# Kernel tuning notes

Hardware: AMD Instinct MI355X
Metric: run time of the kernel (lower is better)

The kernel has to match this reference:

```python
import jax, jax.numpy as jnp
import numpy as np

N_TOKENS = 2048
HIDDEN = 2048
N_EXPERTS = 8
TOP_K = 2
D_FF = 1408  # per-expert SwiGLU intermediate size


def setup_inputs() -> dict:
    key = jax.random.key(0)
    k_h, k_g, k_wg, k_wu, k_wd = jax.random.split(key, 5)
    s_in = 1.0 / np.sqrt(HIDDEN)
    s_ff = 1.0 / np.sqrt(D_FF)
    return {
        "h": jax.random.normal(k_h, (N_TOKENS, HIDDEN), dtype=jnp.float32),
        "gate_w": jax.random.normal(k_g, (N_EXPERTS, HIDDEN), dtype=jnp.float32) * s_in,
        "w_gate": jax.random.normal(k_wg, (N_EXPERTS, HIDDEN, D_FF), dtype=jnp.float32) * s_in,
        "w_up": jax.random.normal(k_wu, (N_EXPERTS, HIDDEN, D_FF), dtype=jnp.float32) * s_in,
        "w_down": jax.random.normal(k_wd, (N_EXPERTS, D_FF, HIDDEN), dtype=jnp.float32) * s_ff,
    }


def reference(h, gate_w, w_gate, w_up, w_down):
    # --- gate: linear (fp32) + softmax + top-k (no renorm, as in source) ---
    logits = jnp.einsum("nd,ed->ne", h.astype(jnp.float32), gate_w.astype(jnp.float32))
    scores = jax.nn.softmax(logits, axis=-1)                 # [N, E]
    topk_weight, topk_idx = jax.lax.top_k(scores, TOP_K)     # [N, K], [N, K]

    # --- per-expert SwiGLU MLP applied densely, then gather selected experts ---
    # (same math as the per-expert grouped GEMM dispatch in the eager loop)
    g = jnp.einsum("nd,edf->enf", h, w_gate)                 # [E, N, F]
    u = jnp.einsum("nd,edf->enf", h, w_up)                   # [E, N, F]
    y = jnp.einsum("enf,efd->end", jax.nn.silu(g) * u, w_down)  # [E, N, D]

    # gather each token's top-k expert outputs: [N, K, D]
    y_tok = jnp.transpose(y, (1, 0, 2))                      # [N, E, D]
    sel = jnp.take_along_axis(y_tok, topk_idx[:, :, None], axis=1)

    # weighted combine
    out = jnp.einsum("nk,nkd->nd", topk_weight.astype(h.dtype), sel)
    return out
```

## Files before the change

### kernel.cpp

```cpp
#include <hip/hip_runtime.h>
#include <hip/hip_bf16.h>
#include <stdint.h>

#define N_TOK 2048
#define HID   2048
#define NEXP  8
#define DFF   1408

typedef __attribute__((ext_vector_type(8))) short short8;
typedef __attribute__((ext_vector_type(4))) float f32x4;

__device__ __forceinline__ unsigned short f2bf(float f) {
  union { float ff; uint32_t u; } v; v.ff = f;
  return (unsigned short)((v.u + 0x7FFFu + ((v.u >> 16) & 1u)) >> 16);
}

__device__ __forceinline__ void gl2lds16(const void* g, void* l) {
  __builtin_amdgcn_global_load_lds(
      (const __attribute__((address_space(1))) void*)g,
      (__attribute__((address_space(3))) void*)l, 16, 0, 0);
}

__global__ __launch_bounds__(256) void gate_topk_k(
    const float* __restrict__ h, const float* __restrict__ gw,
    int* __restrict__ cnt, int* __restrict__ topk_idx, float* __restrict__ topk_w)
{
  int token = blockIdx.x * 4 + (threadIdx.x >> 6);
  int lane  = threadIdx.x & 63;
  const float* hr = h + (size_t)token * HID;
  float acc[NEXP];
#pragma unroll
  for (int e = 0; e < NEXP; ++e) acc[e] = 0.f;
  for (int i = lane; i < HID; i += 64) {
    float hv = hr[i];
#pragma unroll
    for (int e = 0; e < NEXP; ++e) acc[e] = fmaf(hv, gw[e * HID + i], acc[e]);
  }
#pragma unroll
  for (int e = 0; e < NEXP; ++e) {
    float a = acc[e];
#pragma unroll
    for (int s = 32; s > 0; s >>= 1) a += __shfl_xor(a, s, 64);
    acc[e] = a;
  }
  if (lane == 0) {
    float m = acc[0];
#pragma unroll
    for (int e = 1; e < NEXP; ++e) m = fmaxf(m, acc[e]);
    float w[NEXP]; float s = 0.f;
#pragma unroll
    for (int e = 0; e < NEXP; ++e) { w[e] = __expf(acc[e] - m); s += w[e]; }
    float inv = 1.f / s;
    int i0 = 0; float b0 = acc[0];
#pragma unroll
    for (int e = 1; e < NEXP; ++e) if (acc[e] > b0) { b0 = acc[e]; i0 = e; }
    int i1 = -1; float b1 = -3.4e38f;
#pragma unroll
    for (int e = 0; e < NEXP; ++e) if (e != i0 && acc[e] > b1) { b1 = acc[e]; i1 = e; }
    topk_idx[token * 2 + 0] = i0;
    topk_idx[token * 2 + 1] = i1;
    topk_w[token * 2 + 0] = w[i0] * inv;
    topk_w[token * 2 + 1] = w[i1] * inv;
    atomicAdd(&cnt[i0], 1);
    atomicAdd(&cnt[i1], 1);
  }
}

__global__ void prefix_k(const int* __restrict__ cnt, int* __restrict__ offs,
                         int* __restrict__ cursor) {
  if (threadIdx.x == 0 && blockIdx.x == 0) {
    int s = 0;
    for (int e = 0; e < NEXP; ++e) { offs[e] = s; cursor[e] = s; s += cnt[e]; }
  }
}

__global__ __launch_bounds__(256) void scatter_k(
    const int* __restrict__ topk_idx, const float* __restrict__ topk_w,
    int* __restrict__ cursor, int* __restrict__ pair_token, float* __restrict__ pair_w,
    int* __restrict__ tok_slot)
{
  int n = blockIdx.x * 256 + threadIdx.x;
  if (n >= N_TOK) return;
#pragma unroll
  for (int k = 0; k < 2; ++k) {
    int e = topk_idx[n * 2 + k];
    int p = atomicAdd(&cursor[e], 1);
    pair_token[p] = n;
    pair_w[p] = topk_w[n * 2 + k];
    tok_slot[n * 2 + k] = p;
  }
}

__global__ __launch_bounds__(256) void convert_h_k(const float* __restrict__ src,
                                                   unsigned short* __restrict__ dst) {
  int i = blockIdx.x * 256 + threadIdx.x;
  float4 a = ((const float4*)src)[(size_t)i * 2];
  float4 b = ((const float4*)src)[(size_t)i * 2 + 1];
  unsigned short o[8] = {f2bf(a.x), f2bf(a.y), f2bf(a.z), f2bf(a.w),
                         f2bf(b.x), f2bf(b.y), f2bf(b.z), f2bf(b.w)};
  *(short8*)&dst[(size_t)i * 8] = *(const short8*)o;
}

__global__ __launch_bounds__(256) void transpose_k(const float* __restrict__ s1,
                                                   unsigned short* __restrict__ d1,
                                                   const float* __restrict__ s2,
                                                   unsigned short* __restrict__ d2,
                                                   int R, int C, int nz1)
{
  __shared__ unsigned short T[64 * 66];
  const size_t sl = (size_t)R * C;
  int z = blockIdx.z;
  const float* s; unsigned short* d;
  if (z < nz1) { s = s1 + (size_t)z * sl; d = d1 + (size_t)z * sl; }
  else { s = s2 + (size_t)(z - nz1) * sl; d = d2 + (size_t)(z - nz1) * sl; }
  const int rb = blockIdx.x * 64, cb = blockIdx.y * 64;
  const int t = threadIdx.x;
  const int tr = t >> 4, tc = (t & 15) * 4;
  const float* sp = s + (size_t)(rb + tr) * C + cb + tc;
#pragma unroll
  for (int i = 0; i < 4; ++i) {
    float4 v = *(const float4*)(sp + (size_t)i * 16 * C);
    int r = tr + i * 16;
    uint32_t p0 = (uint32_t)f2bf(v.x) | ((uint32_t)f2bf(v.y) << 16);
    uint32_t p1 = (uint32_t)f2bf(v.z) | ((uint32_t)f2bf(v.w) << 16);
    *(uint32_t*)&T[r * 66 + tc]     = p0;
    *(uint32_t*)&T[r * 66 + tc + 2] = p1;
  }
  __syncthreads();
  const int f = t >> 2, ch = (t & 3) * 16;
  unsigned short* dp = d + (size_t)(cb + f) * R + rb + ch;
#pragma unroll
  for (int g = 0; g < 2; ++g) {
    unsigned short buf[8];
#pragma unroll
    for (int j = 0; j < 8; ++j) buf[j] = T[(ch + g * 8 + j) * 66 + f];
    *(short8*)(dp + g * 8) = *(const short8*)buf;
  }
}

__global__ __launch_bounds__(512) void gateup4_k(
    const unsigned short* __restrict__ hbf,
    const unsigned short* __restrict__ wgt, const unsigned short* __restrict__ wut,
    const int* __restrict__ cnt, const int* __restrict__ offs,
    const int* __restrict__ pair_token, unsigned short* __restrict__ act,
    int e_fixed, int nw, int nbcnt, size_t wstride)
{
  const int x = blockIdx.x;
  const int wti = x % nw, mb = x / nw;
  int e, nb;
  if (e_fixed >= 0) { e = e_fixed; nb = wti; }
  else { e = wti / nbcnt; nb = wti % nbcnt; }
  const int count = cnt[e];
  if (mb * 128 >= count) return;
  const int off = offs[e];
  const int rows = min(128, count - mb * 128);
  const int c0 = nb * 128;

  __shared__ unsigned short As[128 * 64];
  __shared__ unsigned short Bg[128 * 64];
  __shared__ unsigned short Bu[128 * 64];
  __shared__ int tok[128];

  const int t = threadIdx.x;
  if (t < 128) tok[t] = pair_token[off + mb * 128 + min(t, rows - 1)];
  __syncthreads();

  const int w = t >> 6, l = t & 63;
  const int sr = l >> 3;
  const int sc = ((l & 7) ^ sr) * 8;
  const int r0 = w * 16 + sr, r1 = w * 16 + 8 + sr;

  const size_t wb = (e_fixed >= 0) ? 0 : (size_t)e * wstride;
  const unsigned short* wgE = wgt + wb;
  const unsigned short* wuE = wut + wb;
  const unsigned short* aP0 = hbf + (size_t)tok[r0] * HID + sc;
  const unsigned short* aP1 = hbf + (size_t)tok[r1] * HID + sc;
  const unsigned short* gP0 = wgE + (size_t)(c0 + r0) * HID + sc;
  const unsigned short* gP1 = wgE + (size_t)(c0 + r1) * HID + sc;
  const unsigned short* uP0 = wuE + (size_t)(c0 + r0) * HID + sc;
  const unsigned short* uP1 = wuE + (size_t)(c0 + r1) * HID + sc;
  const int ldsLo = (w * 16) * 64, ldsHi = (w * 16 + 8) * 64;

  const int fr = l & 15, fq = l >> 4;
  const int wr = (w >> 2) * 64, wc = (w & 3) * 32;
  const int f3 = fr & 7;

  f32x4 accg[4][2], accu[4][2];
#pragma unroll
  for (int i = 0; i < 4; ++i)
#pragma unroll
    for (int j = 0; j < 2; ++j) {
      accg[i][j] = (f32x4){0.f, 0.f, 0.f, 0.f};
      accu[i][j] = (f32x4){0.f, 0.f, 0.f, 0.f};
    }

  for (int kt = 0; kt < HID; kt += 64) {
    gl2lds16(aP0 + kt, &As[ldsLo]); gl2lds16(aP1 + kt, &As[ldsHi]);
    gl2lds16(gP0 + kt, &Bg[ldsLo]); gl2lds16(gP1 + kt, &Bg[ldsHi]);
    gl2lds16(uP0 + kt, &Bu[ldsLo]); gl2lds16(uP1 + kt, &Bu[ldsHi]);
    __syncthreads();

    short8 af[4][2], bg[2][2], bu[2][2];
#pragma unroll
    for (int kk = 0; kk < 2; ++kk) {
      const int ch = ((kk * 4 + fq) ^ f3) * 8;
#pragma unroll
      for (int mi = 0; mi < 4; ++mi)
        af[mi][kk] = *(const short8*)&As[(wr + mi * 16 + fr) * 64 + ch];
#pragma unroll
      for (int ni = 0; ni < 2; ++ni) {
        bg[ni][kk] = *(const short8*)&Bg[(wc + ni * 16 + fr) * 64 + ch];
        bu[ni][kk] = *(const short8*)&Bu[(wc + ni * 16 + fr) * 64 + ch];
      }
    }
#pragma unroll
    for (int kk = 0; kk < 2; ++kk)
#pragma unroll
      for (int mi = 0; mi < 4; ++mi)
#pragma unroll
        for (int ni = 0; ni < 2; ++ni) {
          accg[mi][ni] = __builtin_amdgcn_mfma_f32_16x16x32_bf16(af[mi][kk], bg[ni][kk], accg[mi][ni], 0, 0, 0);
          accu[mi][ni] = __builtin_amdgcn_mfma_f32_16x16x32_bf16(af[mi][kk], bu[ni][kk], accu[mi][ni], 0, 0, 0);
        }
    __syncthreads();
  }

#pragma unroll
  for (int mi = 0; mi < 4; ++mi)
#pragma unroll
    for (int ni = 0; ni < 2; ++ni)
#pragma unroll
      for (int j = 0; j < 4; ++j) {
        int r = wr + mi * 16 + fq * 4 + j;
        if (r < rows) {
          float g = accg[mi][ni][j], u = accu[mi][ni][j];
          float a = (g / (1.f + __expf(-g))) * u;
          act[(size_t)(off + mb * 128 + r) * DFF + (c0 + wc + ni * 16 + fr)] = f2bf(a);
        }
      }
}

__global__ __launch_bounds__(256) void down4_k(
    const unsigned short* __restrict__ act, const unsigned short* __restrict__ wdt,
    const int* __restrict__ cnt, const int* __restrict__ offs,
    float* __restrict__ ypair, int e_fixed, int nw, int nbcnt, size_t wstride)
{
  const int x = blockIdx.x;
  const int wti = x % nw, mb = x / nw;
  int e, nb;
  if (e_fixed >= 0) { e = e_fixed; nb = wti; }
  else { e = wti / nbcnt; nb = wti % nbcnt; }
  const int count = cnt[e];
  if (mb * 128 >= count) return;
  const int off = offs[e];
  const int rows = min(128, count - mb * 128);
  const int c0 = nb * 128;

  __shared__ unsigned short As[128 * 64];
  __shared__ unsigned short Bd[128 * 64];

  const int t = threadIdx.x;
  const int w = t >> 6, l = t & 63;
  const int sr = l >> 3;
  const int sc = ((l & 7) ^ sr) * 8;
  const size_t wb = (e_fixed >= 0) ? 0 : (size_t)e * wstride;
  const unsigned short* wdE = wdt + wb;

  const unsigned short* aP[4];
  const unsigned short* bP[4];
  int ldsB[4];
#pragma unroll
  for (int i = 0; i < 4; ++i) {
    int rr = w * 32 + i * 8 + sr;
    aP[i] = act + (size_t)(off + mb * 128 + rr) * DFF + sc;
    bP[i] = wdE + (size_t)(c0 + rr) * DFF + sc;
    ldsB[i] = (w * 32 + i * 8) * 64;
  }

  const int fr = l & 15, fq = l >> 4;
  const int wr = (w >> 1) * 64, wc = (w & 1) * 64;
  const int f3 = fr & 7;

  f32x4 acc[4][4];
#pragma unroll
  for (int i = 0; i < 4; ++i)
#pragma unroll
    for (int j = 0; j < 4; ++j) acc[i][j] = (f32x4){0.f, 0.f, 0.f, 0.f};

  for (int kt = 0; kt < DFF; kt += 64) {
#pragma unroll
    for (int i = 0; i < 4; ++i) {
      gl2lds16(aP[i] + kt, &As[ldsB[i]]);
      gl2lds16(bP[i] + kt, &Bd[ldsB[i]]);
    }
    __syncthreads();

    short8 af[4][2], bd[4][2];
#pragma unroll
    for (int kk = 0; kk < 2; ++kk) {
      const int ch = ((kk * 4 + fq) ^ f3) * 8;
#pragma unroll
      for (int mi = 0; mi < 4; ++mi)
        af[mi][kk] = *(const short8*)&As[(wr + mi * 16 + fr) * 64 + ch];
#pragma unroll
      for (int ni = 0; ni < 4; ++ni)
        bd[ni][kk] = *(const short8*)&Bd[(wc + ni * 16 + fr) * 64 + ch];
    }
#pragma unroll
    for (int kk = 0; kk < 2; ++kk)
#pragma unroll
      for (int mi = 0; mi < 4; ++mi)
#pragma unroll
        for (int ni = 0; ni < 4; ++ni)
          acc[mi][ni] = __builtin_amdgcn_mfma_f32_16x16x32_bf16(af[mi][kk], bd[ni][kk], acc[mi][ni], 0, 0, 0);
    __syncthreads();
  }

#pragma unroll
  for (int mi = 0; mi < 4; ++mi)
#pragma unroll
    for (int ni = 0; ni < 4; ++ni)
#pragma unroll
      for (int j = 0; j < 4; ++j) {
        int r = wr + mi * 16 + fq * 4 + j;
        if (r < rows)
          ypair[(size_t)(off + mb * 128 + r) * HID + (c0 + wc + ni * 16 + fr)] = acc[mi][ni][j];
      }
}

__global__ __launch_bounds__(256) void combine_k(
    const float* __restrict__ ypair, const int* __restrict__ tok_slot,
    const float* __restrict__ topk_w, float* __restrict__ out)
{
  int i = blockIdx.x * 256 + threadIdx.x;
  int n = i >> (11 - 2);
  int dv = (i & 511) * 4;
  int s0 = tok_slot[n * 2], s1 = tok_slot[n * 2 + 1];
  float w0 = topk_w[n * 2], w1 = topk_w[n * 2 + 1];
  float4 a = *(const float4*)&ypair[(size_t)s0 * HID + dv];
  float4 b = *(const float4*)&ypair[(size_t)s1 * HID + dv];
  float4 o;
  o.x = w0 * a.x + w1 * b.x; o.y = w0 * a.y + w1 * b.y;
  o.z = w0 * a.z + w1 * b.z; o.w = w0 * a.w + w1 * b.w;
  *(float4*)&out[(size_t)n * HID + dv] = o;
}

extern "C" void kernel_launch(void* const* d_in, const int* in_sizes, int n_in,
                              void* d_out, int out_size, void* d_ws, size_t ws_size,
                              hipStream_t stream) {
  const float* h  = (const float*)d_in[0];
  const float* gw = (const float*)d_in[1];
  const float* wg = (const float*)d_in[2];
  const float* wu = (const float*)d_in[3];
  const float* wd = (const float*)d_in[4];
  float* out = (float*)d_out;

  const size_t SL = (size_t)DFF * HID;
  char* ws = (char*)d_ws;
  int*   cnt        = (int*)(ws + 0);
  int*   offs       = (int*)(ws + 32);
  int*   cursor     = (int*)(ws + 64);
  int*   pair_token = (int*)(ws + 256);
  float* pair_w     = (float*)(ws + 16640);
  int*   tok_slot   = (int*)(ws + 33024);
  int*   topk_idx   = (int*)(ws + 49408);
  float* topk_w     = (float*)(ws + 65792);
  unsigned short* act = (unsigned short*)(ws + 82176);
  unsigned short* hbf = (unsigned short*)(ws + 11616512);
  unsigned short* wgt = (unsigned short*)(ws + 20005120);
  unsigned short* wut = (unsigned short*)(ws + 66142464);
  float* ypair_full   = (float*)(ws + 66142464);
  const size_t NEED_FULL = 112279808ull;

  hipMemsetAsync(ws, 0, 256, stream);

  gate_topk_k<<<N_TOK / 4, 256, 0, stream>>>(h, gw, cnt, topk_idx, topk_w);
  prefix_k<<<1, 64, 0, stream>>>(cnt, offs, cursor);
  scatter_k<<<N_TOK / 256, 256, 0, stream>>>(topk_idx, topk_w, cursor, pair_token, pair_w, tok_slot);
  convert_h_k<<<(N_TOK * HID / 8) / 256, 256, 0, stream>>>(h, hbf);

  if (ws_size >= NEED_FULL) {
    transpose_k<<<dim3(HID / 64, DFF / 64, 16), 256, 0, stream>>>(wg, wgt, wu, wut, HID, DFF, 8);
    gateup4_k<<<88 * 16, 512, 0, stream>>>(hbf, wgt, wut, cnt, offs, pair_token, act,
                                           -1, 88, 11, SL);
    transpose_k<<<dim3(DFF / 64, HID / 64, 8), 256, 0, stream>>>(wd, wgt, wd, wgt, DFF, HID, 8);
    down4_k<<<128 * 16, 256, 0, stream>>>(act, wgt, cnt, offs, ypair_full,
                                          -1, 128, 16, SL);
    combine_k<<<(N_TOK * HID / 4) / 256, 256, 0, stream>>>(ypair_full, tok_slot, topk_w, out);
  } else {
    unsigned short* wgtE = (unsigned short*)(ws + 20005120);
    unsigned short* wutE = (unsigned short*)(ws + 25772288);
    float* ypair = (float*)(ws + 31539456);
    for (int e = 0; e < NEXP; ++e) {
      transpose_k<<<dim3(HID / 64, DFF / 64, 2), 256, 0, stream>>>(wg + e * SL, wgtE, wu + e * SL, wutE, HID, DFF, 1);
      gateup4_k<<<11 * 16, 512, 0, stream>>>(hbf, wgtE, wutE, cnt, offs, pair_token, act,
                                             e, 11, 11, 0);
    }
    for (int e = 0; e < NEXP; ++e) {
      transpose_k<<<dim3(DFF / 64, HID / 64, 1), 256, 0, stream>>>(wd + e * SL, wgtE, wd + e * SL, wgtE, DFF, HID, 1);
      down4_k<<<16 * 16, 256, 0, stream>>>(act, wgtE, cnt, offs, ypair, e, 16, 16, 0);
    }
    combine_k<<<(N_TOK * HID / 4) / 256, 256, 0, stream>>>(ypair, tok_slot, topk_w, out);
  }
}
```

Baseline: 329.7 us.

## Double-buffer LDS tiles in grouped GEMM kernels with prefetch and MFMA priority

Both the gate/up and down grouped GEMM kernels now use two LDS buffers per operand. The next K tile is issued via global_load_lds before computing on the current one, with explicit vmcnt waits and barriers replacing __syncthreads. This overlaps global-to-LDS transfer with MFMA work, and s_setprio raises wave priority around the MFMA block. The cost is doubled LDS per block, which may lower occupancy, most notably for the 512-thread gate/up kernel at 96KB.

```diff
diff --git a/kernel.cpp b/kernel.cpp
--- a/kernel.cpp
+++ b/kernel.cpp
@@ -138,7 +138,7 @@
   }
 }
 
-__global__ __launch_bounds__(512) void gateup4_k(
+__global__ __launch_bounds__(512) void gateup5_k(
     const unsigned short* __restrict__ hbf,
     const unsigned short* __restrict__ wgt, const unsigned short* __restrict__ wut,
     const int* __restrict__ cnt, const int* __restrict__ offs,
@@ -156,9 +156,9 @@
   const int rows = min(128, count - mb * 128);
   const int c0 = nb * 128;
 
-  __shared__ unsigned short As[128 * 64];
-  __shared__ unsigned short Bg[128 * 64];
-  __shared__ unsigned short Bu[128 * 64];
+  __shared__ unsigned short As[2][128 * 64];
+  __shared__ unsigned short Bg[2][128 * 64];
+  __shared__ unsigned short Bu[2][128 * 64];
   __shared__ int tok[128];
 
   const int t = threadIdx.x;
@@ -194,25 +194,26 @@
       accu[i][j] = (f32x4){0.f, 0.f, 0.f, 0.f};
     }
 
-  for (int kt = 0; kt < HID; kt += 64) {
-    gl2lds16(aP0 + kt, &As[ldsLo]); gl2lds16(aP1 + kt, &As[ldsHi]);
-    gl2lds16(gP0 + kt, &Bg[ldsLo]); gl2lds16(gP1 + kt, &Bg[ldsHi]);
-    gl2lds16(uP0 + kt, &Bu[ldsLo]); gl2lds16(uP1 + kt, &Bu[ldsHi]);
-    __syncthreads();
-
+  auto stage = [&](int b, int kt) {
+    gl2lds16(aP0 + kt, &As[b][ldsLo]); gl2lds16(aP1 + kt, &As[b][ldsHi]);
+    gl2lds16(gP0 + kt, &Bg[b][ldsLo]); gl2lds16(gP1 + kt, &Bg[b][ldsHi]);
+    gl2lds16(uP0 + kt, &Bu[b][ldsLo]); gl2lds16(uP1 + kt, &Bu[b][ldsHi]);
+  };
+  auto compute = [&](int b) {
     short8 af[4][2], bg[2][2], bu[2][2];
 #pragma unroll
     for (int kk = 0; kk < 2; ++kk) {
       const int ch = ((kk * 4 + fq) ^ f3) * 8;
 #pragma unroll
       for (int mi = 0; mi < 4; ++mi)
-        af[mi][kk] = *(const short8*)&As[(wr + mi * 16 + fr) * 64 + ch];
+        af[mi][kk] = *(const short8*)&As[b][(wr + mi * 16 + fr) * 64 + ch];
 #pragma unroll
       for (int ni = 0; ni < 2; ++ni) {
-        bg[ni][kk] = *(const short8*)&Bg[(wc + ni * 16 + fr) * 64 + ch];
-        bu[ni][kk] = *(const short8*)&Bu[(wc + ni * 16 + fr) * 64 + ch];
+        bg[ni][kk] = *(const short8*)&Bg[b][(wc + ni * 16 + fr) * 64 + ch];
+        bu[ni][kk] = *(const short8*)&Bu[b][(wc + ni * 16 + fr) * 64 + ch];
       }
     }
+    __builtin_amdgcn_s_setprio(1);
 #pragma unroll
     for (int kk = 0; kk < 2; ++kk)
 #pragma unroll
@@ -222,8 +223,23 @@
           accg[mi][ni] = __builtin_amdgcn_mfma_f32_16x16x32_bf16(af[mi][kk], bg[ni][kk], accg[mi][ni], 0, 0, 0);
           accu[mi][ni] = __builtin_amdgcn_mfma_f32_16x16x32_bf16(af[mi][kk], bu[ni][kk], accu[mi][ni], 0, 0, 0);
         }
-    __syncthreads();
-  }
+    __builtin_amdgcn_s_setprio(0);
+  };
+
+  const int NK = HID / 64;
+  stage(0, 0);
+  int cur = 0;
+  for (int k = 0; k + 1 < NK; ++k) {
+    stage(cur ^ 1, (k + 1) * 64);
+    asm volatile("s_waitcnt vmcnt(6)" ::: "memory");
+    asm volatile("s_barrier" ::: "memory");
+    compute(cur);
+    asm volatile("s_barrier" ::: "memory");
+    cur ^= 1;
+  }
+  asm volatile("s_waitcnt vmcnt(0)" ::: "memory");
+  asm volatile("s_barrier" ::: "memory");
+  compute(cur);
 
 #pragma unroll
   for (int mi = 0; mi < 4; ++mi)
@@ -240,7 +256,7 @@
       }
 }
 
-__global__ __launch_bounds__(256) void down4_k(
+__global__ __launch_bounds__(256) void down5_k(
     const unsigned short* __restrict__ act, const unsigned short* __restrict__ wdt,
     const int* __restrict__ cnt, const int* __restrict__ offs,
     float* __restrict__ ypair, int e_fixed, int nw, int nbcnt, size_t wstride)
@@ -256,8 +272,8 @@
   const int rows = min(128, count - mb * 128);
   const int c0 = nb * 128;
 
-  __shared__ unsigned short As[128 * 64];
-  __shared__ unsigned short Bd[128 * 64];
+  __shared__ unsigned short As[2][128 * 64];
+  __shared__ unsigned short Bd[2][128 * 64];
 
   const int t = threadIdx.x;
   const int w = t >> 6, l = t & 63;
@@ -287,25 +303,26 @@
 #pragma unroll
     for (int j = 0; j < 4; ++j) acc[i][j] = (f32x4){0.f, 0.f, 0.f, 0.f};
 
-  for (int kt = 0; kt < DFF; kt += 64) {
+  auto stage = [&](int b, int kt) {
 #pragma unroll
     for (int i = 0; i < 4; ++i) {
-      gl2lds16(aP[i] + kt, &As[ldsB[i]]);
-      gl2lds16(bP[i] + kt, &Bd[ldsB[i]]);
-    }
-    __syncthreads();
-
+      gl2lds16(aP[i] + kt, &As[b][ldsB[i]]);
+      gl2lds16(bP[i] + kt, &Bd[b][ldsB[i]]);
+    }
+  };
+  auto compute = [&](int b) {
     short8 af[4][2], bd[4][2];
 #pragma unroll
     for (int kk = 0; kk < 2; ++kk) {
       const int ch = ((kk * 4 + fq) ^ f3) * 8;
 #pragma unroll
       for (int mi = 0; mi < 4; ++mi)
-        af[mi][kk] = *(const short8*)&As[(wr + mi * 16 + fr) * 64 + ch];
+        af[mi][kk] = *(const short8*)&As[b][(wr + mi * 16 + fr) * 64 + ch];
 #pragma unroll
       for (int ni = 0; ni < 4; ++ni)
-        bd[ni][kk] = *(const short8*)&Bd[(wc + ni * 16 + fr) * 64 + ch];
-    }
+        bd[ni][kk] = *(const short8*)&Bd[b][(wc + ni * 16 + fr) * 64 + ch];
+    }
+    __builtin_amdgcn_s_setprio(1);
 #pragma unroll
     for (int kk = 0; kk < 2; ++kk)
 #pragma unroll
@@ -313,8 +330,23 @@
 #pragma unroll
         for (int ni = 0; ni < 4; ++ni)
           acc[mi][ni] = __builtin_amdgcn_mfma_f32_16x16x32_bf16(af[mi][kk], bd[ni][kk], acc[mi][ni], 0, 0, 0);
-    __syncthreads();
-  }
+    __builtin_amdgcn_s_setprio(0);
+  };
+
+  const int NK = DFF / 64;
+  stage(0, 0);
+  int cur = 0;
+  for (int k = 0; k + 1 < NK; ++k) {
+    stage(cur ^ 1, (k + 1) * 64);
+    asm volatile("s_waitcnt vmcnt(8)" ::: "memory");
+    asm volatile("s_barrier" ::: "memory");
+    compute(cur);
+    asm volatile("s_barrier" ::: "memory");
+    cur ^= 1;
+  }
+  asm volatile("s_waitcnt vmcnt(0)" ::: "memory");
+  asm volatile("s_barrier" ::: "memory");
+  compute(cur);
 
 #pragma unroll
   for (int mi = 0; mi < 4; ++mi)
@@ -333,7 +365,7 @@
     const float* __restrict__ topk_w, float* __restrict__ out)
 {
   int i = blockIdx.x * 256 + threadIdx.x;
-  int n = i >> (11 - 2);
+  int n = i >> 9;
   int dv = (i & 511) * 4;
   int s0 = tok_slot[n * 2], s1 = tok_slot[n * 2 + 1];
   float w0 = topk_w[n * 2], w1 = topk_w[n * 2 + 1];
@@ -381,10 +413,10 @@
 
   if (ws_size >= NEED_FULL) {
     transpose_k<<<dim3(HID / 64, DFF / 64, 16), 256, 0, stream>>>(wg, wgt, wu, wut, HID, DFF, 8);
-    gateup4_k<<<88 * 16, 512, 0, stream>>>(hbf, wgt, wut, cnt, offs, pair_token, act,
+    gateup5_k<<<88 * 16, 512, 0, stream>>>(hbf, wgt, wut, cnt, offs, pair_token, act,
                                            -1, 88, 11, SL);
     transpose_k<<<dim3(DFF / 64, HID / 64, 8), 256, 0, stream>>>(wd, wgt, wd, wgt, DFF, HID, 8);
-    down4_k<<<128 * 16, 256, 0, stream>>>(act, wgt, cnt, offs, ypair_full,
+    down5_k<<<128 * 16, 256, 0, stream>>>(act, wgt, cnt, offs, ypair_full,
                                           -1, 128, 16, SL);
     combine_k<<<(N_TOK * HID / 4) / 256, 256, 0, stream>>>(ypair_full, tok_slot, topk_w, out);
   } else {
@@ -393,12 +425,12 @@
     float* ypair = (float*)(ws + 31539456);
     for (int e = 0; e < NEXP; ++e) {
       transpose_k<<<dim3(HID / 64, DFF / 64, 2), 256, 0, stream>>>(wg + e * SL, wgtE, wu + e * SL, wutE, HID, DFF, 1);
-      gateup4_k<<<11 * 16, 512, 0, stream>>>(hbf, wgtE, wutE, cnt, offs, pair_token, act,
+      gateup5_k<<<11 * 16, 512, 0, stream>>>(hbf, wgtE, wutE, cnt, offs, pair_token, act,
                                              e, 11, 11, 0);
     }
     for (int e = 0; e < NEXP; ++e) {
       transpose_k<<<dim3(DFF / 64, HID / 64, 1), 256, 0, stream>>>(wd + e * SL, wgtE, wd + e * SL, wgtE, DFF, HID, 1);
-      down4_k<<<16 * 16, 256, 0, stream>>>(act, wgtE, cnt, offs, ypair, e, 16, 16, 0);
+      down5_k<<<16 * 16, 256, 0, stream>>>(act, wgtE, cnt, offs, ypair, e, 16, 16, 0);
     }
     combine_k<<<(N_TOK * HID / 4) / 256, 256, 0, stream>>>(ypair, tok_slot, topk_w, out);
   }
```

After: 322.4 us. -2.2%, faster.

## Replace LDS-tiled expert GEMMs with single-wave direct-load MFMA kernels

Applied to the files above, without the earlier changes.

Both grouped GEMMs (gate/up with fused SwiGLU, and down) are rewritten as 64-thread single-wavefront kernels that load MFMA operands straight from global memory into registers. This drops LDS staging and block barriers. Tiles shrink to 64x32 and 64x64 per wave, and each block now loops over several row blocks with stride 8 instead of one block per row tile. This removes shared-memory and sync overhead and raises the number of independent waves, but loses LDS reuse across waves, so global/L2 traffic goes up and the direct loads are uncoalesced 16-byte row-strided accesses.

```diff
diff --git a/kernel.cpp b/kernel.cpp
--- a/kernel.cpp
+++ b/kernel.cpp
@@ -15,11 +15,7 @@
   return (unsigned short)((v.u + 0x7FFFu + ((v.u >> 16) & 1u)) >> 16);
 }
 
-__device__ __forceinline__ void gl2lds16(const void* g, void* l) {
-  __builtin_amdgcn_global_load_lds(
-      (const __attribute__((address_space(1))) void*)g,
-      (__attribute__((address_space(3))) void*)l, 16, 0, 0);
-}
+#define MFMA16(a, b, c) __builtin_amdgcn_mfma_f32_16x16x32_bf16((a), (b), (c), 0, 0, 0)
 
 __global__ __launch_bounds__(256) void gate_topk_k(
     const float* __restrict__ h, const float* __restrict__ gw,
@@ -138,7 +134,7 @@
   }
 }
 
-__global__ __launch_bounds__(512) void gateup4_k(
+__global__ __launch_bounds__(64) void gateup10_k(
     const unsigned short* __restrict__ hbf,
     const unsigned short* __restrict__ wgt, const unsigned short* __restrict__ wut,
     const int* __restrict__ cnt, const int* __restrict__ offs,
@@ -146,186 +142,155 @@
     int e_fixed, int nw, int nbcnt, size_t wstride)
 {
   const int x = blockIdx.x;
-  const int wti = x % nw, mb = x / nw;
+  const int wti = x % nw;
   int e, nb;
   if (e_fixed >= 0) { e = e_fixed; nb = wti; }
   else { e = wti / nbcnt; nb = wti % nbcnt; }
   const int count = cnt[e];
-  if (mb * 128 >= count) return;
   const int off = offs[e];
-  const int rows = min(128, count - mb * 128);
-  const int c0 = nb * 128;
-
-  __shared__ unsigned short As[128 * 64];
-  __shared__ unsigned short Bg[128 * 64];
-  __shared__ unsigned short Bu[128 * 64];
-  __shared__ int tok[128];
-
-  const int t = threadIdx.x;
-  if (t < 128) tok[t] = pair_token[off + mb * 128 + min(t, rows - 1)];
-  __syncthreads();
-
-  const int w = t >> 6, l = t & 63;
-  const int sr = l >> 3;
-  const int sc = ((l & 7) ^ sr) * 8;
-  const int r0 = w * 16 + sr, r1 = w * 16 + 8 + sr;
-
+  const int c0 = nb * 32;
+
+  const int l = threadIdx.x;
+  const int fr = l & 15, fq = l >> 4;
   const size_t wb = (e_fixed >= 0) ? 0 : (size_t)e * wstride;
-  const unsigned short* wgE = wgt + wb;
-  const unsigned short* wuE = wut + wb;
-  const unsigned short* aP0 = hbf + (size_t)tok[r0] * HID + sc;
-  const unsigned short* aP1 = hbf + (size_t)tok[r1] * HID + sc;
-  const unsigned short* gP0 = wgE + (size_t)(c0 + r0) * HID + sc;
-  const unsigned short* gP1 = wgE + (size_t)(c0 + r1) * HID + sc;
-  const unsigned short* uP0 = wuE + (size_t)(c0 + r0) * HID + sc;
-  const unsigned short* uP1 = wuE + (size_t)(c0 + r1) * HID + sc;
-  const int ldsLo = (w * 16) * 64, ldsHi = (w * 16 + 8) * 64;
-
-  const int fr = l & 15, fq = l >> 4;
-  const int wr = (w >> 2) * 64, wc = (w & 3) * 32;
-  const int f3 = fr & 7;
-
-  f32x4 accg[4][2], accu[4][2];
-#pragma unroll
-  for (int i = 0; i < 4; ++i)
-#pragma unroll
-    for (int j = 0; j < 2; ++j) {
-      accg[i][j] = (f32x4){0.f, 0.f, 0.f, 0.f};
-      accu[i][j] = (f32x4){0.f, 0.f, 0.f, 0.f};
-    }
-
-  for (int kt = 0; kt < HID; kt += 64) {
-    gl2lds16(aP0 + kt, &As[ldsLo]); gl2lds16(aP1 + kt, &As[ldsHi]);
-    gl2lds16(gP0 + kt, &Bg[ldsLo]); gl2lds16(gP1 + kt, &Bg[ldsHi]);
-    gl2lds16(uP0 + kt, &Bu[ldsLo]); gl2lds16(uP1 + kt, &Bu[ldsHi]);
-    __syncthreads();
-
-    short8 af[4][2], bg[2][2], bu[2][2];
-#pragma unroll
-    for (int kk = 0; kk < 2; ++kk) {
-      const int ch = ((kk * 4 + fq) ^ f3) * 8;
-#pragma unroll
-      for (int mi = 0; mi < 4; ++mi)
-        af[mi][kk] = *(const short8*)&As[(wr + mi * 16 + fr) * 64 + ch];
-#pragma unroll
-      for (int ni = 0; ni < 2; ++ni) {
-        bg[ni][kk] = *(const short8*)&Bg[(wc + ni * 16 + fr) * 64 + ch];
-        bu[ni][kk] = *(const short8*)&Bu[(wc + ni * 16 + fr) * 64 + ch];
+
+  const unsigned short* bgP0 = wgt + wb + (size_t)(c0 + fr) * HID + fq * 8;
+  const unsigned short* bgP1 = wgt + wb + (size_t)(c0 + 16 + fr) * HID + fq * 8;
+  const unsigned short* buP0 = wut + wb + (size_t)(c0 + fr) * HID + fq * 8;
+  const unsigned short* buP1 = wut + wb + (size_t)(c0 + 16 + fr) * HID + fq * 8;
+
+  for (int mb = x / nw; mb * 64 < count; mb += 8) {
+    const int m0 = mb * 64;
+    const int rows = min(64, count - m0);
+
+    const unsigned short* aP[4];
+#pragma unroll
+    for (int mi = 0; mi < 4; ++mi) {
+      int r = min(m0 + mi * 16 + fr, count - 1);
+      aP[mi] = hbf + (size_t)pair_token[off + r] * HID + fq * 8;
+    }
+
+    f32x4 accg[4][2], accu[4][2];
+#pragma unroll
+    for (int i = 0; i < 4; ++i)
+#pragma unroll
+      for (int j = 0; j < 2; ++j) {
+        accg[i][j] = (f32x4){0.f, 0.f, 0.f, 0.f};
+        accu[i][j] = (f32x4){0.f, 0.f, 0.f, 0.f};
       }
-    }
-#pragma unroll
-    for (int kk = 0; kk < 2; ++kk)
-#pragma unroll
-      for (int mi = 0; mi < 4; ++mi)
-#pragma unroll
-        for (int ni = 0; ni < 2; ++ni) {
-          accg[mi][ni] = __builtin_amdgcn_mfma_f32_16x16x32_bf16(af[mi][kk], bg[ni][kk], accg[mi][ni], 0, 0, 0);
-          accu[mi][ni] = __builtin_amdgcn_mfma_f32_16x16x32_bf16(af[mi][kk], bu[ni][kk], accu[mi][ni], 0, 0, 0);
+
+    for (int kt = 0; kt < HID; kt += 64) {
+      short8 a[4][2], bg[2][2], bu[2][2];
+#pragma unroll
+      for (int kk = 0; kk < 2; ++kk) {
+        const int ko = kt + kk * 32;
+#pragma unroll
+        for (int mi = 0; mi < 4; ++mi)
+          a[mi][kk] = *(const short8*)(aP[mi] + ko);
+        bg[0][kk] = *(const short8*)(bgP0 + ko);
+        bg[1][kk] = *(const short8*)(bgP1 + ko);
+        bu[0][kk] = *(const short8*)(buP0 + ko);
+        bu[1][kk] = *(const short8*)(buP1 + ko);
+      }
+#pragma unroll
+      for (int kk = 0; kk < 2; ++kk)
+#pragma unroll
+        for (int mi = 0; mi < 4; ++mi) {
+          accg[mi][0] = MFMA16(a[mi][kk], bg[0][kk], accg[mi][0]);
+          accg[mi][1] = MFMA16(a[mi][kk], bg[1][kk], accg[mi][1]);
+          accu[mi][0] = MFMA16(a[mi][kk], bu[0][kk], accu[mi][0]);
+          accu[mi][1] = MFMA16(a[mi][kk], bu[1][kk], accu[mi][1]);
         }
-    __syncthreads();
-  }
-
-#pragma unroll
-  for (int mi = 0; mi < 4; ++mi)
-#pragma unroll
-    for (int ni = 0; ni < 2; ++ni)
-#pragma unroll
-      for (int j = 0; j < 4; ++j) {
-        int r = wr + mi * 16 + fq * 4 + j;
-        if (r < rows) {
-          float g = accg[mi][ni][j], u = accu[mi][ni][j];
-          float a = (g / (1.f + __expf(-g))) * u;
-          act[(size_t)(off + mb * 128 + r) * DFF + (c0 + wc + ni * 16 + fr)] = f2bf(a);
+    }
+
+#pragma unroll
+    for (int mi = 0; mi < 4; ++mi)
+#pragma unroll
+      for (int ni = 0; ni < 2; ++ni)
+#pragma unroll
+        for (int j = 0; j < 4; ++j) {
+          int r = mi * 16 + fq * 4 + j;
+          if (r < rows) {
+            float g = accg[mi][ni][j], u = accu[mi][ni][j];
+            float a = (g / (1.f + __expf(-g))) * u;
+            act[(size_t)(off + m0 + r) * DFF + (c0 + ni * 16 + fr)] = f2bf(a);
+          }
         }
-      }
-}
-
-__global__ __launch_bounds__(256) void down4_k(
+  }
+}
+
+__global__ __launch_bounds__(64) void down10_k(
     const unsigned short* __restrict__ act, const unsigned short* __restrict__ wdt,
     const int* __restrict__ cnt, const int* __restrict__ offs,
     float* __restrict__ ypair, int e_fixed, int nw, int nbcnt, size_t wstride)
 {
   const int x = blockIdx.x;
-  const int wti = x % nw, mb = x / nw;
+  const int wti = x % nw;
   int e, nb;
   if (e_fixed >= 0) { e = e_fixed; nb = wti; }
   else { e = wti / nbcnt; nb = wti % nbcnt; }
   const int count = cnt[e];
-  if (mb * 128 >= count) return;
   const int off = offs[e];
-  const int rows = min(128, count - mb * 128);
-  const int c0 = nb * 128;
-
-  __shared__ unsigned short As[128 * 64];
-  __shared__ unsigned short Bd[128 * 64];
-
-  const int t = threadIdx.x;
-  const int w = t >> 6, l = t & 63;
-  const int sr = l >> 3;
-  const int sc = ((l & 7) ^ sr) * 8;
+  const int c0 = nb * 64;
+
+  const int l = threadIdx.x;
+  const int fr = l & 15, fq = l >> 4;
   const size_t wb = (e_fixed >= 0) ? 0 : (size_t)e * wstride;
-  const unsigned short* wdE = wdt + wb;
-
-  const unsigned short* aP[4];
-  const unsigned short* bP[4];
-  int ldsB[4];
-#pragma unroll
-  for (int i = 0; i < 4; ++i) {
-    int rr = w * 32 + i * 8 + sr;
-    aP[i] = act + (size_t)(off + mb * 128 + rr) * DFF + sc;
-    bP[i] = wdE + (size_t)(c0 + rr) * DFF + sc;
-    ldsB[i] = (w * 32 + i * 8) * 64;
-  }
-
-  const int fr = l & 15, fq = l >> 4;
-  const int wr = (w >> 1) * 64, wc = (w & 1) * 64;
-  const int f3 = fr & 7;
-
-  f32x4 acc[4][4];
-#pragma unroll
-  for (int i = 0; i < 4; ++i)
-#pragma unroll
-    for (int j = 0; j < 4; ++j) acc[i][j] = (f32x4){0.f, 0.f, 0.f, 0.f};
-
-  for (int kt = 0; kt < DFF; kt += 64) {
-#pragma unroll
-    for (int i = 0; i < 4; ++i) {
-      gl2lds16(aP[i] + kt, &As[ldsB[i]]);
-      gl2lds16(bP[i] + kt, &Bd[ldsB[i]]);
-    }
-    __syncthreads();
-
-    short8 af[4][2], bd[4][2];
-#pragma unroll
-    for (int kk = 0; kk < 2; ++kk) {
-      const int ch = ((kk * 4 + fq) ^ f3) * 8;
-#pragma unroll
-      for (int mi = 0; mi < 4; ++mi)
-        af[mi][kk] = *(const short8*)&As[(wr + mi * 16 + fr) * 64 + ch];
+
+  const unsigned short* bdP[4];
+#pragma unroll
+  for (int ni = 0; ni < 4; ++ni)
+    bdP[ni] = wdt + wb + (size_t)(c0 + ni * 16 + fr) * DFF + fq * 8;
+
+  for (int mb = x / nw; mb * 64 < count; mb += 8) {
+    const int m0 = mb * 64;
+    const int rows = min(64, count - m0);
+
+    const unsigned short* aP[4];
+#pragma unroll
+    for (int mi = 0; mi < 4; ++mi) {
+      int r = min(m0 + mi * 16 + fr, count - 1);
+      aP[mi] = act + (size_t)(off + r) * DFF + fq * 8;
+    }
+
+    f32x4 acc[4][4];
+#pragma unroll
+    for (int i = 0; i < 4; ++i)
+#pragma unroll
+      for (int j = 0; j < 4; ++j) acc[i][j] = (f32x4){0.f, 0.f, 0.f, 0.f};
+
+    for (int kt = 0; kt < DFF; kt += 64) {
+      short8 a[4][2], bd[4][2];
+#pragma unroll
+      for (int kk = 0; kk < 2; ++kk) {
+        const int ko = kt + kk * 32;
+#pragma unroll
+        for (int mi = 0; mi < 4; ++mi)
+          a[mi][kk] = *(const short8*)(aP[mi] + ko);
+#pragma unroll
+        for (int ni = 0; ni < 4; ++ni)
+          bd[ni][kk] = *(const short8*)(bdP[ni] + ko);
+      }
+#pragma unroll
+      for (int kk = 0; kk < 2; ++kk)
+#pragma unroll
+        for (int mi = 0; mi < 4; ++mi)
+#pragma unroll
+          for (int ni = 0; ni < 4; ++ni)
+            acc[mi][ni] = MFMA16(a[mi][kk], bd[ni][kk], acc[mi][ni]);
+    }
+
+#pragma unroll
+    for (int mi = 0; mi < 4; ++mi)
 #pragma unroll
       for (int ni = 0; ni < 4; ++ni)
-        bd[ni][kk] = *(const short8*)&Bd[(wc + ni * 16 + fr) * 64 + ch];
-    }
-#pragma unroll
-    for (int kk = 0; kk < 2; ++kk)
-#pragma unroll
-      for (int mi = 0; mi < 4; ++mi)
-#pragma unroll
-        for (int ni = 0; ni < 4; ++ni)
-          acc[mi][ni] = __builtin_amdgcn_mfma_f32_16x16x32_bf16(af[mi][kk], bd[ni][kk], acc[mi][ni], 0, 0, 0);
-    __syncthreads();
-  }
-
-#pragma unroll
-  for (int mi = 0; mi < 4; ++mi)
-#pragma unroll
-    for (int ni = 0; ni < 4; ++ni)
-#pragma unroll
-      for (int j = 0; j < 4; ++j) {
-        int r = wr + mi * 16 + fq * 4 + j;
-        if (r < rows)
-          ypair[(size_t)(off + mb * 128 + r) * HID + (c0 + wc + ni * 16 + fr)] = acc[mi][ni][j];
-      }
+#pragma unroll
+        for (int j = 0; j < 4; ++j) {
+          int r = mi * 16 + fq * 4 + j;
+          if (r < rows)
+            ypair[(size_t)(off + m0 + r) * HID + (c0 + ni * 16 + fr)] = acc[mi][ni][j];
+        }
+  }
 }
 
 __global__ __launch_bounds__(256) void combine_k(
@@ -333,7 +298,7 @@
     const float* __restrict__ topk_w, float* __restrict__ out)
 {
   int i = blockIdx.x * 256 + threadIdx.x;
-  int n = i >> (11 - 2);
+  int n = i >> 9;
   int dv = (i & 511) * 4;
   int s0 = tok_slot[n * 2], s1 = tok_slot[n * 2 + 1];
   float w0 = topk_w[n * 2], w1 = topk_w[n * 2 + 1];
@@ -381,11 +346,11 @@
 
   if (ws_size >= NEED_FULL) {
     transpose_k<<<dim3(HID / 64, DFF / 64, 16), 256, 0, stream>>>(wg, wgt, wu, wut, HID, DFF, 8);
-    gateup4_k<<<88 * 16, 512, 0, stream>>>(hbf, wgt, wut, cnt, offs, pair_token, act,
-                                           -1, 88, 11, SL);
+    gateup10_k<<<352 * 8, 64, 0, stream>>>(hbf, wgt, wut, cnt, offs, pair_token, act,
+                                           -1, 352, 44, SL);
     transpose_k<<<dim3(DFF / 64, HID / 64, 8), 256, 0, stream>>>(wd, wgt, wd, wgt, DFF, HID, 8);
-    down4_k<<<128 * 16, 256, 0, stream>>>(act, wgt, cnt, offs, ypair_full,
-                                          -1, 128, 16, SL);
+    down10_k<<<256 * 8, 64, 0, stream>>>(act, wgt, cnt, offs, ypair_full,
+                                         -1, 256, 32, SL);
     combine_k<<<(N_TOK * HID / 4) / 256, 256, 0, stream>>>(ypair_full, tok_slot, topk_w, out);
   } else {
     unsigned short* wgtE = (unsigned short*)(ws + 20005120);
@@ -393,12 +358,12 @@
     float* ypair = (float*)(ws + 31539456);
     for (int e = 0; e < NEXP; ++e) {
       transpose_k<<<dim3(HID / 64, DFF / 64, 2), 256, 0, stream>>>(wg + e * SL, wgtE, wu + e * SL, wutE, HID, DFF, 1);
-      gateup4_k<<<11 * 16, 512, 0, stream>>>(hbf, wgtE, wutE, cnt, offs, pair_token, act,
-                                             e, 11, 11, 0);
+      gateup10_k<<<44 * 8, 64, 0, stream>>>(hbf, wgtE, wutE, cnt, offs, pair_token, act,
+                                            e, 44, 44, 0);
     }
     for (int e = 0; e < NEXP; ++e) {
       transpose_k<<<dim3(DFF / 64, HID / 64, 1), 256, 0, stream>>>(wd + e * SL, wgtE, wd + e * SL, wgtE, DFF, HID, 1);
-      down4_k<<<16 * 16, 256, 0, stream>>>(act, wgtE, cnt, offs, ypair, e, 16, 16, 0);
+      down10_k<<<32 * 8, 64, 0, stream>>>(act, wgtE, cnt, offs, ypair, e, 32, 32, 0);
     }
     combine_k<<<(N_TOK * HID / 4) / 256, 256, 0, stream>>>(ypair, tok_slot, topk_w, out);
   }
```

Result: slower. 506.4 us (+53.6%).
